# Kernel tuning notes

Measured on AMD Instinct MI355X. Metric: run time of the kernel, lower is better.

## Reference

```python
import jax, jax.numpy as jnp
import numpy as np

MIN_BIN = 3.25
MAX_BIN = 20.75
NUM_BINS = 15
INF = 100000000.0
N = 1536
D_PAIR = 128

def setup_inputs() -> dict:
    key = jax.random.key(0)
    k1, k2, k3 = jax.random.split(key, 3)
    x = jax.random.normal(k1, (N, 3), dtype=jnp.float32)
    W = jax.random.normal(k2, (D_PAIR, NUM_BINS), dtype=jnp.float32)
    b = jax.random.normal(k3, (D_PAIR,), dtype=jnp.float32)
    return {"x": x, "W": W, "b": b}

def reference(x, W, b):
    # squared bin edges, like torch.linspace(min,max,num_bins)**2
    bins = jnp.linspace(MIN_BIN, MAX_BIN, NUM_BINS, dtype=jnp.float32) ** 2  # [num_bins]
    upper = jnp.concatenate([bins[1:], jnp.array([INF], dtype=jnp.float32)])  # [num_bins]
    # pairwise squared distances: [N, N, 1]
    d = jnp.sum((x[:, None, :] - x[None, :, :]) ** 2, axis=-1, keepdims=True)
    # one-hot binning: strictly greater than lower edge, strictly less than upper edge
    oh = ((d > bins) & (d < upper)).astype(W.dtype)  # [N, N, num_bins]
    # linear projection: [N, N, d_pair]
    return jnp.einsum('ijk,pk->ijp', oh, W) + b
```

## Files before the change

kernel.cpp:

```cpp
#include <hip/hip_runtime.h>


#define NBINS 15
#define NPTS  1536
#define DPAIR 128
#define JSPLIT 2
#define JCHUNK (NPTS / JSPLIT)
#define CHUNK_F4 (JCHUNK * DPAIR / 4)

typedef float f32x4 __attribute__((ext_vector_type(4)));

__global__ __launch_bounds__(256, 8) void recycling_embedder_kernel(
    const float* __restrict__ x,
    const float* __restrict__ W,
    const float* __restrict__ b,
    float* __restrict__ out) {
    __shared__ float table[16 * DPAIR];
    __shared__ unsigned short offs[JCHUNK];

    const int i    = blockIdx.x >> 1;
    const int half = blockIdx.x & 1;
    const int t    = threadIdx.x;

    float bins[NBINS];
#pragma unroll
    for (int k = 0; k < NBINS; ++k) {
        float e = 3.25f + 1.25f * (float)k;
        bins[k] = e * e;
    }

    for (int e = t; e < 16 * DPAIR; e += 256) {
        int row = e >> 7;
        int p   = e & (DPAIR - 1);
        float v = b[p];
        if (row > 0) v += W[p * NBINS + (row - 1)];
        table[e] = v;
    }

    const float xi0 = x[i * 3 + 0];
    const float xi1 = x[i * 3 + 1];
    const float xi2 = x[i * 3 + 2];
    const int j0 = half * JCHUNK;
    for (int jj = t; jj < JCHUNK; jj += 256) {
        int j = j0 + jj;
        float d;
        {
#pragma clang fp contract(off)
            float dx = xi0 - x[j * 3 + 0];
            float dy = xi1 - x[j * 3 + 1];
            float dz = xi2 - x[j * 3 + 2];
            d = dx * dx + dy * dy + dz * dz;
        }
        int cnt = 0, eq = 0;
#pragma unroll
        for (int k = 0; k < NBINS; ++k) {
            cnt += (d > bins[k]) ? 1 : 0;
            eq  |= (d == bins[k]) ? 1 : 0;
        }
        int idx = eq ? 0 : cnt;
        offs[jj] = (unsigned short)(idx * (DPAIR / 4));
    }
    __syncthreads();

    const f32x4* table4 = (const f32x4*)table;
    f32x4* ochunk = (f32x4*)out
                  + (size_t)i * (NPTS * DPAIR / 4)
                  + (size_t)(j0 * (DPAIR / 4));
#pragma unroll 4
    for (int l = t; l < CHUNK_F4; l += 256) {
        int jj     = l >> 5;
        int within = l & 31;
        ochunk[l] = table4[offs[jj] + within];
    }
}

extern "C" void kernel_launch(void* const* d_in, const int* in_sizes, int n_in,
                              void* d_out, int out_size, void* d_ws, size_t ws_size,
                              hipStream_t stream) {
    const float* x = (const float*)d_in[0];
    const float* W = (const float*)d_in[1];
    const float* b = (const float*)d_in[2];
    float* out = (float*)d_out;

    dim3 grid(NPTS * JSPLIT), block(256);
    recycling_embedder_kernel<<<grid, block, 0, stream>>>(x, W, b, out);
}
```

Measured before the change: 1.159 ms.

## Split into prep kernel for bin indices and grid-stride streaming store kernel

Adds a prep kernel that writes the 16-row bias+W table and a per-pair byte bin index into workspace. A second persistent-style kernel with a fixed 2048-block grid then streams the output by gathering table rows from global memory (cached) via the index array. This removes the per-block table rebuild and shared-memory sync from the store path, at the cost of an extra launch and an extra read of the index array. It only runs when the workspace is large enough, otherwise it falls back to the old kernel.

```diff
diff --git a/kernel.cpp b/kernel.cpp
--- a/kernel.cpp
+++ b/kernel.cpp
@@ -4,13 +4,89 @@
 #define NBINS 15
 #define NPTS  1536
 #define DPAIR 128
+#define NPAIR (NPTS * NPTS)
+#define TOT_F4 (NPAIR * (DPAIR / 4))
+#define SBLOCKS 2048
+#define NT (SBLOCKS * 256)
+#define NITER (TOT_F4 / NT)
+
+#define TAB_BYTES (16 * DPAIR * 4)
+#define WS_NEEDED (TAB_BYTES + NPAIR)
+
+typedef float f32x4 __attribute__((ext_vector_type(4)));
+
+__global__ __launch_bounds__(256) void prep_kernel(
+    const float* __restrict__ x,
+    const float* __restrict__ W,
+    const float* __restrict__ b,
+    float* __restrict__ tab,
+    unsigned char* __restrict__ idx) {
+    const int i = blockIdx.x;
+    const int t = threadIdx.x;
+
+    float bins[NBINS];
+#pragma unroll
+    for (int k = 0; k < NBINS; ++k) {
+        float e = 3.25f + 1.25f * (float)k;
+        bins[k] = e * e;
+    }
+
+    if (i == 0) {
+        for (int e = t; e < 16 * DPAIR; e += 256) {
+            int row = e >> 7;
+            int p   = e & (DPAIR - 1);
+            float v = b[p];
+            if (row > 0) v += W[p * NBINS + (row - 1)];
+            tab[e] = v;
+        }
+    }
+
+    const float xi0 = x[i * 3 + 0];
+    const float xi1 = x[i * 3 + 1];
+    const float xi2 = x[i * 3 + 2];
+    for (int j = t; j < NPTS; j += 256) {
+        float d;
+        {
+#pragma clang fp contract(off)
+            float dx = xi0 - x[j * 3 + 0];
+            float dy = xi1 - x[j * 3 + 1];
+            float dz = xi2 - x[j * 3 + 2];
+            d = dx * dx + dy * dy + dz * dz;
+        }
+        int cnt = 0, eq = 0;
+#pragma unroll
+        for (int k = 0; k < NBINS; ++k) {
+            cnt += (d > bins[k]) ? 1 : 0;
+            eq  |= (d == bins[k]) ? 1 : 0;
+        }
+        idx[i * NPTS + j] = (unsigned char)(eq ? 0 : cnt);
+    }
+}
+
+__global__ __launch_bounds__(256, 8) void stream_kernel(
+    const float* __restrict__ tab,
+    const unsigned char* __restrict__ idx,
+    float* __restrict__ out) {
+    const f32x4* tab4 = (const f32x4*)tab;
+    f32x4* out4 = (f32x4*)out;
+
+    const unsigned flat = blockIdx.x * 256u + threadIdx.x;
+    const unsigned w = flat & 31u;
+
+#pragma unroll 4
+    for (int it = 0; it < NITER; ++it) {
+        unsigned g = flat + (unsigned)it * (unsigned)NT;
+        unsigned p = g >> 5;
+        unsigned id = idx[p];
+        out4[g] = tab4[id * 32u + w];
+    }
+}
+
 #define JSPLIT 2
 #define JCHUNK (NPTS / JSPLIT)
 #define CHUNK_F4 (JCHUNK * DPAIR / 4)
 
-typedef float f32x4 __attribute__((ext_vector_type(4)));
-
-__global__ __launch_bounds__(256, 8) void recycling_embedder_kernel(
+__global__ __launch_bounds__(256, 8) void recycling_embedder_fallback(
     const float* __restrict__ x,
     const float* __restrict__ W,
     const float* __restrict__ b,
@@ -57,8 +133,8 @@
             cnt += (d > bins[k]) ? 1 : 0;
             eq  |= (d == bins[k]) ? 1 : 0;
         }
-        int idx = eq ? 0 : cnt;
-        offs[jj] = (unsigned short)(idx * (DPAIR / 4));
+        int bidx = eq ? 0 : cnt;
+        offs[jj] = (unsigned short)(bidx * (DPAIR / 4));
     }
     __syncthreads();
 
@@ -82,6 +158,14 @@
     const float* b = (const float*)d_in[2];
     float* out = (float*)d_out;
 
-    dim3 grid(NPTS * JSPLIT), block(256);
-    recycling_embedder_kernel<<<grid, block, 0, stream>>>(x, W, b, out);
+    if (ws_size >= (size_t)WS_NEEDED && d_ws != nullptr) {
+        float* tab = (float*)d_ws;
+        unsigned char* idx = (unsigned char*)d_ws + TAB_BYTES;
+
+        prep_kernel<<<dim3(NPTS), dim3(256), 0, stream>>>(x, W, b, tab, idx);
+        stream_kernel<<<dim3(SBLOCKS), dim3(256), 0, stream>>>(tab, idx, out);
+    } else {
+        recycling_embedder_fallback<<<dim3(NPTS * JSPLIT), dim3(256), 0, stream>>>(
+            x, W, b, out);
+    }
 }
```

New measurement: 1.206 ms. +4.0%, slower.

## Hold bin lookup table in registers and select rows with a bitwise mux tree

Applied to the files above, without the earlier changes.

Each thread now preloads all 16 rows of the bias+weight table, for its fixed 16-byte column, from shared memory into registers. It then picks the output row per pair with a 4-level select tree driven by the bin index bits. This replaces the per-store shared-memory gather. Bin indices are stored as bytes in a transposed layout, so each wave reads eight indices at once as a uint2. The aim is to remove LDS traffic and address arithmetic from the store loop. The cost is about 60 conditional moves per 16-byte store, higher register pressure, and a minimum occupancy hint lowered from 8 to 4 blocks.

```diff
diff --git a/kernel.cpp b/kernel.cpp
--- a/kernel.cpp
+++ b/kernel.cpp
@@ -6,17 +6,26 @@
 #define DPAIR 128
 #define JSPLIT 2
 #define JCHUNK (NPTS / JSPLIT)
-#define CHUNK_F4 (JCHUNK * DPAIR / 4)
+#define NPACK  12
 
 typedef float f32x4 __attribute__((ext_vector_type(4)));
 
-__global__ __launch_bounds__(256, 8) void recycling_embedder_kernel(
+static __device__ __forceinline__ f32x4 sel(int c, f32x4 a, f32x4 b) {
+    f32x4 r;
+    r[0] = c ? a[0] : b[0];
+    r[1] = c ? a[1] : b[1];
+    r[2] = c ? a[2] : b[2];
+    r[3] = c ? a[3] : b[3];
+    return r;
+}
+
+__global__ __launch_bounds__(256, 4) void recycling_embedder_kernel(
     const float* __restrict__ x,
     const float* __restrict__ W,
     const float* __restrict__ b,
     float* __restrict__ out) {
-    __shared__ float table[16 * DPAIR];
-    __shared__ unsigned short offs[JCHUNK];
+    __shared__ __align__(16) float table[16 * DPAIR];
+    __shared__ __align__(8) unsigned char idsT[8 * 96];
 
     const int i    = blockIdx.x >> 1;
     const int half = blockIdx.x & 1;
@@ -57,21 +66,81 @@
             cnt += (d > bins[k]) ? 1 : 0;
             eq  |= (d == bins[k]) ? 1 : 0;
         }
-        int idx = eq ? 0 : cnt;
-        offs[jj] = (unsigned short)(idx * (DPAIR / 4));
+        idsT[(jj & 7) * 96 + (jj >> 3)] = (unsigned char)(eq ? 0 : cnt);
     }
     __syncthreads();
 
-    const f32x4* table4 = (const f32x4*)table;
-    f32x4* ochunk = (f32x4*)out
-                  + (size_t)i * (NPTS * DPAIR / 4)
-                  + (size_t)(j0 * (DPAIR / 4));
-#pragma unroll 4
-    for (int l = t; l < CHUNK_F4; l += 256) {
-        int jj     = l >> 5;
-        int within = l & 31;
-        ochunk[l] = table4[offs[jj] + within];
+    const char* tabc = (const char*)table;
+    const int wb = (t & 31) * 16;
+    f32x4 t0  = *(const f32x4*)(tabc +  0 * 512 + wb);
+    f32x4 t1  = *(const f32x4*)(tabc +  1 * 512 + wb);
+    f32x4 t2  = *(const f32x4*)(tabc +  2 * 512 + wb);
+    f32x4 t3  = *(const f32x4*)(tabc +  3 * 512 + wb);
+    f32x4 t4  = *(const f32x4*)(tabc +  4 * 512 + wb);
+    f32x4 t5  = *(const f32x4*)(tabc +  5 * 512 + wb);
+    f32x4 t6  = *(const f32x4*)(tabc +  6 * 512 + wb);
+    f32x4 t7  = *(const f32x4*)(tabc +  7 * 512 + wb);
+    f32x4 t8  = *(const f32x4*)(tabc +  8 * 512 + wb);
+    f32x4 t9  = *(const f32x4*)(tabc +  9 * 512 + wb);
+    f32x4 t10 = *(const f32x4*)(tabc + 10 * 512 + wb);
+    f32x4 t11 = *(const f32x4*)(tabc + 11 * 512 + wb);
+    f32x4 t12 = *(const f32x4*)(tabc + 12 * 512 + wb);
+    f32x4 t13 = *(const f32x4*)(tabc + 13 * 512 + wb);
+    f32x4 t14 = *(const f32x4*)(tabc + 14 * 512 + wb);
+    f32x4 t15 = *(const f32x4*)(tabc + 15 * 512 + wb);
+
+    const unsigned char* idcol = &idsT[(t >> 5) * 96];
+    f32x4* pout = (f32x4*)out
+                + (size_t)i * (NPTS * DPAIR / 4)
+                + (size_t)(j0 * (DPAIR / 4))
+                + t;
+
+#define SELECT(idv, dst) do {                                              \
+        int b0_ = (idv) & 1, b1_ = (idv) & 2, b2_ = (idv) & 4,             \
+            b3_ = (idv) & 8;                                               \
+        f32x4 a0_ = sel(b0_, t1,  t0),  a1_ = sel(b0_, t3,  t2);           \
+        f32x4 a2_ = sel(b0_, t5,  t4),  a3_ = sel(b0_, t7,  t6);           \
+        f32x4 a4_ = sel(b0_, t9,  t8),  a5_ = sel(b0_, t11, t10);          \
+        f32x4 a6_ = sel(b0_, t13, t12), a7_ = sel(b0_, t15, t14);          \
+        f32x4 c0_ = sel(b1_, a1_, a0_), c1_ = sel(b1_, a3_, a2_);          \
+        f32x4 c2_ = sel(b1_, a5_, a4_), c3_ = sel(b1_, a7_, a6_);          \
+        f32x4 d0_ = sel(b2_, c1_, c0_), d1_ = sel(b2_, c3_, c2_);          \
+        dst = sel(b3_, d1_, d0_);                                          \
+    } while (0)
+
+#define ITER(word, sh, u) do {                                             \
+        int id_ = ((word) >> (sh)) & 15;                                   \
+        f32x4 v_;                                                          \
+        SELECT(id_, v_);                                                   \
+        pout[(u) * 256] = v_;                                              \
+    } while (0)
+
+#define PROC(PK) do {                                                      \
+        unsigned lo_ = (PK).x, hi_ = (PK).y;                               \
+        ITER(lo_,  0, 0); ITER(lo_,  8, 1);                                \
+        ITER(lo_, 16, 2); ITER(lo_, 24, 3);                                \
+        ITER(hi_,  0, 4); ITER(hi_,  8, 5);                                \
+        ITER(hi_, 16, 6); ITER(hi_, 24, 7);                                \
+        pout += 8 * 256;                                                   \
+    } while (0)
+
+    uint2 pA = *(const uint2*)(idcol + 0 * 8);
+#pragma unroll 1
+    for (int k = 0; k < NPACK - 2; k += 2) {
+        uint2 pB = *(const uint2*)(idcol + (k + 1) * 8);
+        PROC(pA);
+        pA = *(const uint2*)(idcol + (k + 2) * 8);
+        PROC(pB);
     }
+    {
+        uint2 pB = *(const uint2*)(idcol + (NPACK - 1) * 8);
+        PROC(pA);
+        PROC(pB);
+    }
+
+#undef SELECT
+#undef ITER
+#undef PROC
 }
 
 extern "C" void kernel_launch(void* const* d_in, const int* in_sizes, int n_in,
```

Result: slower. 1.473 ms (+27.1%).
